# Kernel optimization log

Measured on AMD Instinct MI355X. Metric: run time of the kernel, lower is better.

## Reference

```python
import jax, jax.numpy as jnp
import numpy as np

B, T, K, D = 32, 1000, 512, 512


def setup_inputs() -> dict:
    key = jax.random.key(0)
    ks = jax.random.split(key, 10)
    s = lambda k, shape: jax.random.normal(k, shape, jnp.float32) * 0.05
    return {
        "zi": jax.random.randint(ks[0], (B, T), 0, K),
        "c": jax.random.normal(ks[1], (B, D, T), jnp.float32),
        "emb": s(ks[2], (K, D)),
        "W1": s(ks[3], (2 * D, D)), "b1": jnp.zeros((D,), jnp.float32),
        "W2": s(ks[4], (D, D)), "b2": jnp.zeros((D,), jnp.float32),
        "W_ih": s(ks[5], (D, 4 * D)), "b_ih": jnp.zeros((4 * D,), jnp.float32),
        "W_hh": s(ks[6], (D, 4 * D)), "b_hh": jnp.zeros((4 * D,), jnp.float32),
        "W_out": s(ks[7], (D, K)), "b_out": jnp.zeros((K,), jnp.float32),
    }


def reference(zi, c, emb, W1, b1, W2, b2, W_ih, b_ih, W_hh, b_hh, W_out, b_out):
    Bb, Tt = zi.shape
    Dd = emb.shape[1]
    # teacher-forced inputs: embed and shift right by one (pad with zeros)
    z = emb[zi]                                                    # [B,T,D]
    z_prev = jnp.concatenate([jnp.zeros((Bb, 1, Dd), z.dtype), z[:, :-1]], axis=1)
    x = jnp.concatenate([z_prev, jnp.transpose(c, (0, 2, 1))], axis=-1)  # [B,T,2D]
    # prenet has no sequential dependence -> batch over all timesteps
    pre = jax.nn.relu(x @ W1 + b1) @ W2 + b2                       # [B,T,D]
    # precompute the input-to-hidden gate contribution for all steps
    xg = jnp.transpose(pre @ W_ih + b_ih + b_hh, (1, 0, 2))        # [T,B,4D]

    def step(carry, gx):
        h, cc = carry
        gates = gx + h @ W_hh                                      # [B,4D]
        i, f, g, o = jnp.split(gates, 4, axis=-1)                  # torch LSTMCell order
        i = jax.nn.sigmoid(i)
        f = jax.nn.sigmoid(f)
        g = jnp.tanh(g)
        o = jax.nn.sigmoid(o)
        cc = f * cc + i * g
        h = o * jnp.tanh(cc)
        return (h, cc), h

    h0 = jnp.zeros((Bb, Dd), pre.dtype)
    _, hs = jax.lax.scan(step, (h0, h0), xg)                       # [T,B,D]
    logits = hs @ W_out + b_out                                    # [T,B,K]
    return jnp.transpose(logits, (1, 2, 0))                        # [B,K,T]
```

## Files before the change

kernel.cpp:

```cpp
#include <hip/hip_runtime.h>
#include <stdint.h>

typedef unsigned short u16;
typedef unsigned int u32;
typedef unsigned long long u64;
typedef __attribute__((ext_vector_type(8))) short bh8;
typedef __attribute__((ext_vector_type(8))) unsigned short u16x8;
typedef __attribute__((ext_vector_type(4))) float f32x4;
typedef __attribute__((ext_vector_type(4))) unsigned int u32x4;

#define B_ 32
#define T_ 1000
#define D_ 512
#define NG 2048

__device__ __forceinline__ float bf2f(u16 u) {
  union { unsigned int i; float f; } v; v.i = ((unsigned int)u) << 16; return v.f;
}
__device__ __forceinline__ u16 f2bf(float f) {
  union { float f; unsigned int i; } v; v.f = f;
  return (u16)((v.i + 0x7fffu + ((v.i >> 16) & 1u)) >> 16);
}

__global__ __launch_bounds__(256) void wtrans_k(const float* __restrict__ src,
                                                u16* __restrict__ dst, int R, int C) {
  __shared__ float tile[32][33];
  const int r0 = blockIdx.x * 32, c0 = blockIdx.y * 32;
  const int tid = threadIdx.x;
#pragma unroll
  for (int q = 0; q < 4; q++) {
    int idx = q * 256 + tid, rr = idx >> 5, cc = idx & 31;
    tile[rr][cc] = src[(size_t)(r0 + rr) * C + c0 + cc];
  }
  __syncthreads();
#pragma unroll
  for (int q = 0; q < 4; q++) {
    int idx = q * 256 + tid, cc = idx >> 5, rr = idx & 31;
    dst[(size_t)(c0 + cc) * R + r0 + rr] = f2bf(tile[rr][cc]);
  }
}

__global__ void bsum_k(const float* __restrict__ a, const float* __restrict__ b,
                       float* __restrict__ o) {
  int i = blockIdx.x * blockDim.x + threadIdx.x;
  if (i < NG) o[i] = a[i] + b[i];
}

__global__ __launch_bounds__(256) void embed_k(const int* __restrict__ zi,
                                               const float* __restrict__ emb,
                                               u16* __restrict__ x) {
  const int tid = threadIdx.x;
  const int r = blockIdx.x * 4 + (tid >> 6);
  const int d0 = (tid & 63) * 8;
  const int t = r >> 5, b = r & 31;
  u16x8 o;
  if (t == 0) {
#pragma unroll
    for (int i = 0; i < 8; i++) o[i] = 0;
  } else {
    const int zv = zi[b * T_ + t - 1];
    const float* s = emb + (size_t)zv * D_ + d0;
#pragma unroll
    for (int i = 0; i < 8; i++) o[i] = f2bf(s[i]);
  }
  *(u16x8*)(x + (size_t)r * 1024 + d0) = o;
}

__global__ __launch_bounds__(256) void ctrans_k(const float* __restrict__ c,
                                                u16* __restrict__ x) {
  __shared__ float tile[32][65];
  const int b = blockIdx.z, d0 = blockIdx.y * 32, t0 = blockIdx.x * 64;
  const int tid = threadIdx.x;
  const int dd = tid >> 3, tt0 = (tid & 7) * 8;
  const float* src = c + ((size_t)b * D_ + d0 + dd) * T_ + t0 + tt0;
#pragma unroll
  for (int i = 0; i < 8; i++) {
    int tt = tt0 + i;
    tile[dd][tt] = (t0 + tt < T_) ? src[i] : 0.f;
  }
  __syncthreads();
  const int tt = tid & 63, dq = tid >> 6;
  if (t0 + tt < T_) {
    u16x8 o;
#pragma unroll
    for (int i = 0; i < 8; i++) o[i] = f2bf(tile[dq * 8 + i][tt]);
    *(u16x8*)(x + ((size_t)(t0 + tt) * 32 + b) * 1024 + 512 + d0 + dq * 8) = o;
  }
}

template <bool RELU, bool SCATTER>
__global__ __launch_bounds__(256, 2) void gemm_k(const u16* __restrict__ A,
                                                 const u16* __restrict__ Bt,
                                                 const float* __restrict__ bias,
                                                 void* __restrict__ Cout,
                                                 int M, int N, int K) {
  __shared__ u16 Al[128 * 40];
  __shared__ u16 Bl[128 * 40];
  const int tid = threadIdx.x;
  const int w = tid >> 6, l = tid & 63;
  const int row0 = blockIdx.x * 128, col0 = blockIdx.y * 128;
  const int wr = (w >> 1) * 64, wc = (w & 1) * 64;
  f32x4 acc[4][4];
  const f32x4 zero = {0.f, 0.f, 0.f, 0.f};
#pragma unroll
  for (int i = 0; i < 4; i++)
#pragma unroll
    for (int j = 0; j < 4; j++) acc[i][j] = zero;

  const int sm = tid >> 2;
  const int sk = (tid & 3) * 8;
  const u16* Ap = A + (size_t)(row0 + sm) * K + sk;
  const u16* Bp = Bt + (size_t)(col0 + sm) * K + sk;
  const size_t half = (size_t)64 * K;
  const int ldo = sm * 40 + sk;
  const int lr = l & 15, lk = (l >> 4) * 8;
  const int KT = K >> 5;

  bh8 a0 = *(const bh8*)Ap, a1 = *(const bh8*)(Ap + half);
  bh8 b0 = *(const bh8*)Bp, b1 = *(const bh8*)(Bp + half);

  for (int kt = 0; kt < KT; kt++) {
    const int kn = (kt + 1 < KT) ? (kt + 1) * 32 : 0;
    bh8 na0 = *(const bh8*)(Ap + kn), na1 = *(const bh8*)(Ap + half + kn);
    bh8 nb0 = *(const bh8*)(Bp + kn), nb1 = *(const bh8*)(Bp + half + kn);
    *(bh8*)(Al + ldo) = a0;
    *(bh8*)(Al + ldo + 64 * 40) = a1;
    *(bh8*)(Bl + ldo) = b0;
    *(bh8*)(Bl + ldo + 64 * 40) = b1;
    __syncthreads();
    bh8 af[4], bfr[4];
#pragma unroll
    for (int i = 0; i < 4; i++) af[i] = *(const bh8*)(Al + (wr + i * 16 + lr) * 40 + lk);
#pragma unroll
    for (int j = 0; j < 4; j++) bfr[j] = *(const bh8*)(Bl + (wc + j * 16 + lr) * 40 + lk);
#pragma unroll
    for (int i = 0; i < 4; i++)
#pragma unroll
      for (int j = 0; j < 4; j++)
        acc[i][j] = __builtin_amdgcn_mfma_f32_16x16x32_bf16(af[i], bfr[j], acc[i][j], 0, 0, 0);
    __syncthreads();
    a0 = na0; a1 = na1; b0 = nb0; b1 = nb1;
  }

  const int lrow = (l >> 4) * 4;
#pragma unroll
  for (int j = 0; j < 4; j++) {
    const int n = col0 + wc + j * 16 + lr;
    const float bv = bias[n];
#pragma unroll
    for (int i = 0; i < 4; i++) {
      const int r = row0 + wr + i * 16 + lrow;
      if (SCATTER) {
        const int bb = r / T_;
        const int t = r - bb * T_;
        f32x4 o;
#pragma unroll
        for (int e = 0; e < 4; e++) o[e] = acc[i][j][e] + bv;
        *(f32x4*)((float*)Cout + ((size_t)bb * N + n) * T_ + t) = o;
      } else {
#pragma unroll
        for (int e = 0; e < 4; e++) {
          float v = acc[i][j][e] + bv;
          if (RELU) v = v > 0.f ? v : 0.f;
          ((u16*)Cout)[(size_t)(r + e) * N + n] = f2bf(v);
        }
      }
    }
  }
}

__global__ __launch_bounds__(256, 1) void scan_k(const u16* __restrict__ xg,
                                                 const u16* __restrict__ Whht,
                                                 u16* __restrict__ hs,
                                                 u32* hbuf) {
  __shared__ u16 hstage[16 * 552];
  __shared__ float gl[4 * 132];
  const int tid = threadIdx.x;
  const int wgid = blockIdx.x;
  const int grp = wgid & 7;
  const int wgin = wgid >> 3;
  if (wgin >= 16) return;
  const int D0 = wgin * 32;
  const int w = tid >> 6, l = tid & 63;
  const int lr = l & 15, lc = l >> 4;
  const int aoff = lc * 136 + lr * 8;

  u32* fb = hbuf;
  u32* sb = hbuf + 32768;

  bh8 bfr[2][16];
#pragma unroll
  for (int j = 0; j < 2; j++) {
    const int c = w * 512 + D0 + j * 16 + lr;
    const u16* wp = Whht + (size_t)c * 512 + lc * 8;
#pragma unroll
    for (int kk = 0; kk < 16; kk++) bfr[j][kk] = *(const bh8*)(wp + kk * 32);
  }

  for (int i = tid; i < 16 * 552 / 2; i += 256) ((u32*)hstage)[i] = 0u;

  const int pb = tid >> 5, pd = tid & 31;
  const int gbat = grp * 4 + pb;
  const int gdim = D0 + pd;
  float ccv = 0.f;
  u16 xh0[4], xh1[4];
  if (tid < 128) {
    const u16* xp0 = xg + (size_t)gbat * NG + gdim;
    const u16* xp1 = xg + ((size_t)32 + gbat) * NG + gdim;
#pragma unroll
    for (int g = 0; g < 4; g++) { xh0[g] = xp0[g * 512]; xh1[g] = xp1[g * 512]; }
  }
  const int rb = tid >> 6;
  const int rd0 = (tid & 63) * 8;
  const int stidx = (rd0 >> 5) * 552 + ((rd0 >> 3) & 3) * 136 + rb * 8;
  bool slowmode = false;
  __syncthreads();

  auto step = [&](const int t, u16 (&xh)[4]) {
    f32x4 a0 = {0.f, 0.f, 0.f, 0.f}, a1 = a0;
#pragma unroll
    for (int kk = 0; kk < 16; kk++) {
      bh8 af = *(const bh8*)(hstage + kk * 552 + aoff);
      a0 = __builtin_amdgcn_mfma_f32_16x16x32_bf16(af, bfr[0][kk], a0, 0, 0, 0);
      a1 = __builtin_amdgcn_mfma_f32_16x16x32_bf16(af, bfr[1][kk], a1, 0, 0, 0);
    }
    if (lc == 0) {
#pragma unroll
      for (int e = 0; e < 4; e++) {
        gl[e * 132 + w * 32 + lr] = a0[e];
        gl[e * 132 + w * 32 + 16 + lr] = a1[e];
      }
    }
    asm volatile("s_waitcnt lgkmcnt(0)\n\ts_barrier" ::: "memory");
    __builtin_amdgcn_sched_barrier(0);

    u16 hb = 0;
    if (tid < 128) {
      const float gi = gl[pb * 132 + pd]      + bf2f(xh[0]);
      const float gf = gl[pb * 132 + 32 + pd] + bf2f(xh[1]);
      const float gg = gl[pb * 132 + 64 + pd] + bf2f(xh[2]);
      const float go = gl[pb * 132 + 96 + pd] + bf2f(xh[3]);
      const float si = 1.f / (1.f + __expf(-gi));
      const float sf = 1.f / (1.f + __expf(-gf));
      const float tg = 1.f - 2.f / (__expf(2.f * gg) + 1.f);
      const float so = 1.f / (1.f + __expf(-go));
      ccv = sf * ccv + si * tg;
      const float hv = so * (1.f - 2.f / (__expf(2.f * ccv) + 1.f));
      hb = f2bf(hv);
      if (t + 1 < T_) {
        const u32 tagged = ((u32)(t + 1) << 16) | (u32)hb;
        const size_t idx = ((size_t)((t & 1) * 8 + grp) * 4 + pb) * 512 + gdim;
        asm volatile("global_store_dword %0, %1, off sc0"
                     :: "v"((u64)(uintptr_t)(fb + idx)), "v"(tagged) : "memory");
        (void)__hip_atomic_exchange(sb + idx, tagged, __ATOMIC_RELAXED,
                                    __HIP_MEMORY_SCOPE_AGENT);
      }
    }
    if (t + 1 < T_) {
      const u32 tag = (u32)(t + 1);
      const size_t base = ((size_t)((t & 1) * 8 + grp) * 4 + rb) * 512 + rd0;
      const u64 pa = (u64)(uintptr_t)(fb + base);
      u32x4 qa, qb;
      if (!slowmode) {
        int rounds = 0;
        for (;;) {
          asm volatile("global_load_dwordx4 %0, %2, off sc0\n\t"
                       "global_load_dwordx4 %1, %2, off offset:16 sc0\n\t"
                       "s_waitcnt vmcnt(0)"
                       : "=&v"(qa), "=&v"(qb) : "v"(pa) : "memory");
          const bool bad = (qa[0] >> 16) != tag || (qa[1] >> 16) != tag ||
                           (qa[2] >> 16) != tag || (qa[3] >> 16) != tag ||
                           (qb[0] >> 16) != tag || (qb[1] >> 16) != tag ||
                           (qb[2] >> 16) != tag || (qb[3] >> 16) != tag;
          if (!__ballot(bad)) break;
          if (++rounds > 512) { slowmode = true; break; }
        }
      }
      if (slowmode) {
        const u64* sp = (const u64*)(sb + base);
        for (;;) {
          u64 s0 = __hip_atomic_load(sp + 0, __ATOMIC_RELAXED, __HIP_MEMORY_SCOPE_AGENT);
          u64 s1 = __hip_atomic_load(sp + 1, __ATOMIC_RELAXED, __HIP_MEMORY_SCOPE_AGENT);
          u64 s2 = __hip_atomic_load(sp + 2, __ATOMIC_RELAXED, __HIP_MEMORY_SCOPE_AGENT);
          u64 s3 = __hip_atomic_load(sp + 3, __ATOMIC_RELAXED, __HIP_MEMORY_SCOPE_AGENT);
          qa[0] = (u32)s0; qa[1] = (u32)(s0 >> 32);
          qa[2] = (u32)s1; qa[3] = (u32)(s1 >> 32);
          qb[0] = (u32)s2; qb[1] = (u32)(s2 >> 32);
          qb[2] = (u32)s3; qb[3] = (u32)(s3 >> 32);
          const bool bad = (qa[0] >> 16) != tag || (qa[1] >> 16) != tag ||
                           (qa[2] >> 16) != tag || (qa[3] >> 16) != tag ||
                           (qb[0] >> 16) != tag || (qb[1] >> 16) != tag ||
                           (qb[2] >> 16) != tag || (qb[3] >> 16) != tag;
          if (!__ballot(bad)) break;
        }
      }
      u32x4 pw;
      pw[0] = (qa[0] & 0xffffu) | (qa[1] << 16);
      pw[1] = (qa[2] & 0xffffu) | (qa[3] << 16);
      pw[2] = (qb[0] & 0xffffu) | (qb[1] << 16);
      pw[3] = (qb[2] & 0xffffu) | (qb[3] << 16);
      *(u32x4*)(hstage + stidx) = pw;
    }
    if (tid < 128) {
      hs[((size_t)gbat * T_ + t) * 512 + gdim] = hb;
      if (t + 2 < T_) {
        const u16* xp = xg + ((size_t)(t + 2) * 32 + gbat) * NG + gdim;
#pragma unroll
        for (int g = 0; g < 4; g++) xh[g] = xp[g * 512];
      }
    }
    asm volatile("s_waitcnt lgkmcnt(0)\n\ts_barrier" ::: "memory");
    __builtin_amdgcn_sched_barrier(0);
  };

  for (int t = 0; t < T_; t += 2) {
    step(t, xh0);
    step(t + 1, xh1);
  }
}

extern "C" void kernel_launch(void* const* d_in, const int* in_sizes, int n_in,
                              void* d_out, int out_size, void* d_ws, size_t ws_size,
                              hipStream_t stream) {
  const int*   zi    = (const int*)d_in[0];
  const float* c     = (const float*)d_in[1];
  const float* emb   = (const float*)d_in[2];
  const float* W1    = (const float*)d_in[3];
  const float* b1    = (const float*)d_in[4];
  const float* W2    = (const float*)d_in[5];
  const float* b2    = (const float*)d_in[6];
  const float* W_ih  = (const float*)d_in[7];
  const float* b_ih  = (const float*)d_in[8];
  const float* W_hh  = (const float*)d_in[9];
  const float* b_hh  = (const float*)d_in[10];
  const float* W_out = (const float*)d_in[11];
  const float* b_out = (const float*)d_in[12];
  float* out = (float*)d_out;
  char* ws = (char*)d_ws;

  const size_t x_off   = 0;
  const size_t xg_off  = 65536000;
  const size_t pre_off = 32768000;
  const size_t w_off   = xg_off + 131072000;
  u16* xb    = (u16*)(ws + x_off);
  u16* hsb   = (u16*)(ws + x_off);
  u16* preb  = (u16*)(ws + pre_off);
  u16* xgb   = (u16*)(ws + xg_off);
  u16* h1b   = (u16*)(ws + xg_off);
  u16* W1t   = (u16*)(ws + w_off);
  u16* W2t   = W1t + 512 * 1024;
  u16* Wiht  = W2t + 512 * 512;
  u16* Whht  = Wiht + 2048 * 512;
  u16* Woutt = Whht + 2048 * 512;
  float* bsum = (float*)(Woutt + 512 * 512);
  u32* hbuf  = (u32*)(bsum + NG);

  hipMemsetAsync(hbuf, 0, 2 * 32768 * sizeof(u32), stream);

  wtrans_k<<<dim3(32, 16), 256, 0, stream>>>(W1, W1t, 1024, 512);
  wtrans_k<<<dim3(16, 16), 256, 0, stream>>>(W2, W2t, 512, 512);
  wtrans_k<<<dim3(16, 64), 256, 0, stream>>>(W_ih, Wiht, 512, 2048);
  wtrans_k<<<dim3(16, 64), 256, 0, stream>>>(W_hh, Whht, 512, 2048);
  wtrans_k<<<dim3(16, 16), 256, 0, stream>>>(W_out, Woutt, 512, 512);
  bsum_k<<<8, 256, 0, stream>>>(b_ih, b_hh, bsum);
  embed_k<<<8000, 256, 0, stream>>>(zi, emb, xb);
  ctrans_k<<<dim3(16, 16, 32), 256, 0, stream>>>(c, xb);

  gemm_k<true,  false><<<dim3(250, 4),  256, 0, stream>>>(xb,   W1t,   b1,    h1b,  32000, 512,  1024);
  gemm_k<false, false><<<dim3(250, 4),  256, 0, stream>>>(h1b,  W2t,   b2,    preb, 32000, 512,  512);
  gemm_k<false, false><<<dim3(250, 16), 256, 0, stream>>>(preb, Wiht,  bsum,  xgb,  32000, 2048, 512);
  scan_k<<<256, 256, 0, stream>>>(xgb, Whht, hsb, hbuf);
  gemm_k<false, true ><<<dim3(250, 4),  256, 0, stream>>>(hsb,  Woutt, b_out, out,  32000, 512,  512);
}
```

Baseline: 2.886 ms.

## Remap W_hh columns per wave so gate activations stay in registers, drop LDS barrier

Result: faster. 2.776 ms, median of 2 (-3.8%).

```diff
diff --git a/kernel.cpp b/kernel.cpp
--- a/kernel.cpp
+++ b/kernel.cpp
@@ -173,8 +173,7 @@
                                                  const u16* __restrict__ Whht,
                                                  u16* __restrict__ hs,
                                                  u32* hbuf) {
-  __shared__ u16 hstage[16 * 552];
-  __shared__ float gl[4 * 132];
+  __shared__ u16 hstage[2][16 * 552];
   const int tid = threadIdx.x;
   const int wgid = blockIdx.x;
   const int grp = wgid & 7;
@@ -184,6 +183,7 @@
   const int w = tid >> 6, l = tid & 63;
   const int lr = l & 15, lc = l >> 4;
   const int aoff = lc * 136 + lr * 8;
+  const int Dw = D0 + 8 * w;
 
   u32* fb = hbuf;
   u32* sb = hbuf + 32768;
@@ -191,74 +191,96 @@
   bh8 bfr[2][16];
 #pragma unroll
   for (int j = 0; j < 2; j++) {
-    const int c = w * 512 + D0 + j * 16 + lr;
-    const u16* wp = Whht + (size_t)c * 512 + lc * 8;
+    const int gate = 2 * j + (lr >> 3);
+    const u16* wp = Whht + (size_t)(gate * 512 + Dw + (lr & 7)) * 512 + lc * 8;
 #pragma unroll
     for (int kk = 0; kk < 16; kk++) bfr[j][kk] = *(const bh8*)(wp + kk * 32);
   }
 
-  for (int i = tid; i < 16 * 552 / 2; i += 256) ((u32*)hstage)[i] = 0u;
-
-  const int pb = tid >> 5, pd = tid & 31;
-  const int gbat = grp * 4 + pb;
-  const int gdim = D0 + pd;
-  float ccv = 0.f;
-  u16 xh0[4], xh1[4];
-  if (tid < 128) {
-    const u16* xp0 = xg + (size_t)gbat * NG + gdim;
-    const u16* xp1 = xg + ((size_t)32 + gbat) * NG + gdim;
-#pragma unroll
-    for (int g = 0; g < 4; g++) { xh0[g] = xp0[g * 512]; xh1[g] = xp1[g * 512]; }
+  for (int i = tid; i < 8832; i += 256) ((u32*)hstage)[i] = 0u;
+
+  const int gdim = Dw + (l & 7);
+  const int eb = (l >> 3) & 1 ? 2 : 0;
+  float cc2[2] = {0.f, 0.f};
+  u16 xh0[2][4], xh1[2][4];
+  if (l < 16) {
+#pragma unroll
+    for (int j = 0; j < 2; j++) {
+      const int gb = grp * 4 + eb + j;
+#pragma unroll
+      for (int g = 0; g < 4; g++) {
+        xh0[j][g] = xg[(size_t)gb * NG + g * 512 + gdim];
+        xh1[j][g] = xg[((size_t)32 + gb) * NG + g * 512 + gdim];
+      }
+    }
   }
   const int rb = tid >> 6;
   const int rd0 = (tid & 63) * 8;
-  const int stidx = (rd0 >> 5) * 552 + ((rd0 >> 3) & 3) * 136 + rb * 8;
+  const int stbase = (rd0 >> 5) * 552 + ((rd0 >> 3) & 3) * 136 + rb * 8;
   bool slowmode = false;
   __syncthreads();
 
-  auto step = [&](const int t, u16 (&xh)[4]) {
+  auto step = [&](const int t, u16 (&xh)[2][4]) {
+    const int cur = t & 1;
     f32x4 a0 = {0.f, 0.f, 0.f, 0.f}, a1 = a0;
 #pragma unroll
     for (int kk = 0; kk < 16; kk++) {
-      bh8 af = *(const bh8*)(hstage + kk * 552 + aoff);
+      bh8 af = *(const bh8*)(&hstage[cur][kk * 552 + aoff]);
       a0 = __builtin_amdgcn_mfma_f32_16x16x32_bf16(af, bfr[0][kk], a0, 0, 0, 0);
       a1 = __builtin_amdgcn_mfma_f32_16x16x32_bf16(af, bfr[1][kk], a1, 0, 0, 0);
     }
-    if (lc == 0) {
-#pragma unroll
-      for (int e = 0; e < 4; e++) {
-        gl[e * 132 + w * 32 + lr] = a0[e];
-        gl[e * 132 + w * 32 + 16 + lr] = a1[e];
-      }
-    }
-    asm volatile("s_waitcnt lgkmcnt(0)\n\ts_barrier" ::: "memory");
-    __builtin_amdgcn_sched_barrier(0);
-
-    u16 hb = 0;
-    if (tid < 128) {
-      const float gi = gl[pb * 132 + pd]      + bf2f(xh[0]);
-      const float gf = gl[pb * 132 + 32 + pd] + bf2f(xh[1]);
-      const float gg = gl[pb * 132 + 64 + pd] + bf2f(xh[2]);
-      const float go = gl[pb * 132 + 96 + pd] + bf2f(xh[3]);
-      const float si = 1.f / (1.f + __expf(-gi));
-      const float sf = 1.f / (1.f + __expf(-gf));
-      const float tg = 1.f - 2.f / (__expf(2.f * gg) + 1.f);
-      const float so = 1.f / (1.f + __expf(-go));
-      ccv = sf * ccv + si * tg;
-      const float hv = so * (1.f - 2.f / (__expf(2.f * ccv) + 1.f));
-      hb = f2bf(hv);
+    f32x4 b0, b1;
+#pragma unroll
+    for (int e = 0; e < 4; e++) {
+      b0[e] = __shfl_xor(a0[e], 8);
+      b1[e] = __shfl_xor(a1[e], 8);
+    }
+    if (l < 16) {
+      const bool hi = (l >> 3) & 1;
+      const f32x4 vi = hi ? b0 : a0, vf = hi ? a0 : b0;
+      const f32x4 vg = hi ? b1 : a1, vo = hi ? a1 : b1;
+      u16 hbv[2];
+#pragma unroll
+      for (int j = 0; j < 2; j++) {
+        const int e = eb + j;
+        const float gi = vi[e] + bf2f(xh[j][0]);
+        const float gf = vf[e] + bf2f(xh[j][1]);
+        const float gg = vg[e] + bf2f(xh[j][2]);
+        const float go = vo[e] + bf2f(xh[j][3]);
+        const float si = 1.f / (1.f + __expf(-gi));
+        const float sf = 1.f / (1.f + __expf(-gf));
+        const float tg = 1.f - 2.f / (__expf(2.f * gg) + 1.f);
+        const float so = 1.f / (1.f + __expf(-go));
+        cc2[j] = sf * cc2[j] + si * tg;
+        hbv[j] = f2bf(so * (1.f - 2.f / (__expf(2.f * cc2[j]) + 1.f)));
+      }
       if (t + 1 < T_) {
-        const u32 tagged = ((u32)(t + 1) << 16) | (u32)hb;
-        const size_t idx = ((size_t)((t & 1) * 8 + grp) * 4 + pb) * 512 + gdim;
-        asm volatile("global_store_dword %0, %1, off sc0"
-                     :: "v"((u64)(uintptr_t)(fb + idx)), "v"(tagged) : "memory");
-        (void)__hip_atomic_exchange(sb + idx, tagged, __ATOMIC_RELAXED,
-                                    __HIP_MEMORY_SCOPE_AGENT);
+        const u32 tag = (u32)(t + 1) << 16;
+#pragma unroll
+        for (int j = 0; j < 2; j++) {
+          const size_t idx = ((size_t)(cur * 8 + grp) * 4 + eb + j) * 512 + gdim;
+          const u32 tv = tag | (u32)hbv[j];
+          asm volatile("global_store_dword %0, %2, off sc0\n\t"
+                       "global_store_dword %1, %2, off sc1"
+                       :: "v"((u64)(uintptr_t)(fb + idx)), "v"((u64)(uintptr_t)(sb + idx)),
+                          "v"(tv) : "memory");
+        }
+      }
+#pragma unroll
+      for (int j = 0; j < 2; j++)
+        hs[((size_t)(grp * 4 + eb + j) * T_ + t) * 512 + gdim] = hbv[j];
+      if (t + 2 < T_) {
+#pragma unroll
+        for (int j = 0; j < 2; j++) {
+          const u16* xp = xg + ((size_t)(t + 2) * 32 + grp * 4 + eb + j) * NG + gdim;
+#pragma unroll
+          for (int g = 0; g < 4; g++) xh[j][g] = xp[g * 512];
+        }
       }
     }
     if (t + 1 < T_) {
       const u32 tag = (u32)(t + 1);
-      const size_t base = ((size_t)((t & 1) * 8 + grp) * 4 + rb) * 512 + rd0;
+      const size_t base = ((size_t)(cur * 8 + grp) * 4 + rb) * 512 + rd0;
       const u64 pa = (u64)(uintptr_t)(fb + base);
       u32x4 qa, qb;
       if (!slowmode) {
@@ -299,15 +321,7 @@
       pw[1] = (qa[2] & 0xffffu) | (qa[3] << 16);
       pw[2] = (qb[0] & 0xffffu) | (qb[1] << 16);
       pw[3] = (qb[2] & 0xffffu) | (qb[3] << 16);
-      *(u32x4*)(hstage + stidx) = pw;
-    }
-    if (tid < 128) {
-      hs[((size_t)gbat * T_ + t) * 512 + gdim] = hb;
-      if (t + 2 < T_) {
-        const u16* xp = xg + ((size_t)(t + 2) * 32 + gbat) * NG + gdim;
-#pragma unroll
-        for (int g = 0; g < 4; g++) xh[g] = xp[g * 512];
-      }
+      *(u32x4*)(&hstage[cur ^ 1][stbase]) = pw;
     }
     asm volatile("s_waitcnt lgkmcnt(0)\n\ts_barrier" ::: "memory");
     __builtin_amdgcn_sched_barrier(0);
```
